# Kernel tuning notes

Measured on AMD Instinct MI355X. Metric: run time of the kernel, lower is better.

Reference implementation:

```python
import jax, jax.numpy as jnp
import numpy as np

NUM_SENSORS = 128
ANGLE = 0.5235987755982988  # 30 degrees
# delay_samples[s] = round(s * c/(2*fs) * sin(angle)/c * fs) = round(s*sin(angle)/2)

def _delay_samples(num_sensors):
    pos_scaled = np.arange(num_sensors) * np.sin(ANGLE) / 2.0
    return jnp.asarray(np.round(pos_scaled).astype(np.int32))


def setup_inputs() -> dict:
    key = jax.random.key(0)
    B, T, S = 16, 100000, NUM_SENSORS
    microphone_array = jax.random.normal(key, (B, T, S), dtype=jnp.float32)
    return {"microphone_array": microphone_array}


def reference(microphone_array):
    B, T, S = microphone_array.shape
    d = _delay_samples(S)                      # [S] int32, per-sensor shift
    t = jnp.arange(T, dtype=jnp.int32)
    idx = t[:, None] + d[None, :]              # [T, S] source sample index
    valid = idx < T                            # zero-pad past the end
    idx_c = jnp.minimum(idx, T - 1)
    # gather shifted signal per sensor: shifted[b, t, s] = x[b, t + d_s, s]
    gidx = jnp.broadcast_to(idx_c[None, :, :], (B, T, S))
    shifted = jnp.take_along_axis(microphone_array, gidx, axis=1)
    shifted = jnp.where(valid[None, :, :], shifted, jnp.zeros((), microphone_array.dtype))
    return jnp.sum(shifted, axis=-1) / S       # [B, T]
```

## Files before the change

### kernel.cpp

```cpp
#include <hip/hip_runtime.h>
#include <math.h>


#define SENS 128

#define FTT   224
#define FROWS (FTT + 32)
#define FRSTR (FTT + 2)
#define FNSLOT 33

__global__ __launch_bounds__(256, 5)
void das3_kernel(const float* __restrict__ x, float* __restrict__ out, int T) {
    __shared__ float P[FNSLOT * FRSTR];

    const int tid = threadIdx.x;
    const int b   = blockIdx.y;
    const int t0  = blockIdx.x * FTT;
    const int L   = tid & 31;
    const int rb  = tid >> 5;

    const int s0 = 4 * L - (L > 0);
    const float* __restrict__ xrow  = x + (size_t)b * (size_t)T * SENS + s0;
    const float* __restrict__ xlast = x + (size_t)b * (size_t)T * SENS + (SENS - 1);

    float* __restrict__ Pw  = P + L * FRSTR - L;
    float* __restrict__ PwE = P + 32 * FRSTR - 32;

    if (t0 + FROWS <= T) {
        #pragma unroll
        for (int bb = 0; bb < 4; ++bb) {
            float4 v[8];
            float  vl[8];
            #pragma unroll
            for (int k = 0; k < 8; ++k) {
                const int r = (bb * 8 + k) * 8 + rb;
                v[k] = *(const float4*)(xrow + (size_t)(t0 + r) * SENS);
            }
            if (L == 31) {
                #pragma unroll
                for (int k = 0; k < 8; ++k) {
                    const int r = (bb * 8 + k) * 8 + rb;
                    vl[k] = xlast[(size_t)(t0 + r) * SENS];
                }
            }
            #pragma unroll
            for (int k = 0; k < 8; ++k) {
                const int r = (bb * 8 + k) * 8 + rb;
                const float4 q = v[k];
                const float R = q.x + q.y + q.z + (L ? q.w : 0.0f);
                if (r >= L && r < L + FTT) Pw[r] = R;
                if (L == 31 && r >= 32)    PwE[r] = vl[k];
            }
        }
    } else {
        for (int i = tid; i < FNSLOT * FRSTR; i += 256) P[i] = 0.0f;
        __syncthreads();
        for (int sw = 0; sw < FROWS / 8; ++sw) {
            const int r = sw * 8 + rb;
            const int u = t0 + r;
            if (u < T) {
                const float4 q = *(const float4*)(xrow + (size_t)u * SENS);
                const float R = q.x + q.y + q.z + (L ? q.w : 0.0f);
                if (r >= L && r < L + FTT) Pw[r] = R;
                if (L == 31 && r >= 32)    PwE[r] = xlast[(size_t)u * SENS];
            }
        }
    }
    __syncthreads();

    const int t = t0 + tid;
    if (tid < FTT && t < T) {
        float acc = 0.0f;
        #pragma unroll
        for (int j = 0; j < FNSLOT; ++j)
            acc += P[j * FRSTR + tid];
        out[(size_t)b * T + t] = acc * (1.0f / SENS);
    }
}

#define TT   256
#define ROWS (TT + 32)
#define RSTR (ROWS + 1)
#define NSLOT 64

struct Tabs {
    int off[NSLOT];
    unsigned cm1, cm2, cm3;
};

__global__ __launch_bounds__(256)
void das2_kernel(const float* __restrict__ x, float* __restrict__ out,
                 Tabs tb, int T) {
    __shared__ float P[NSLOT * RSTR];

    const int tid = threadIdx.x;
    const int b   = blockIdx.y;
    const int t0  = blockIdx.x * TT;

    const int L = tid & 31;
    const bool c1 = (tb.cm1 >> L) & 1u;
    const bool c2 = (tb.cm2 >> L) & 1u;
    const bool c3 = (tb.cm3 >> L) & 1u;
    const int rb = tid >> 5;
    float* __restrict__ Pw = P + (2 * L) * RSTR;
    const float* __restrict__ xb = x + (size_t)b * (size_t)T * SENS + 4 * L;

    if (t0 + ROWS <= T) {
        #pragma unroll 4
        for (int sw = 0; sw < ROWS / 8; ++sw) {
            const int r = sw * 8 + rb;
            const float4 v = *(const float4*)(xb + (size_t)(t0 + r) * SENS);
            float a = v.x;
            a += c1 ? v.y : 0.0f;
            a += c2 ? v.z : 0.0f;
            a += c3 ? v.w : 0.0f;
            const float g = (c1 ? 0.0f : v.y) + (c2 ? 0.0f : v.z)
                          + (c3 ? 0.0f : v.w);
            Pw[r]        = a;
            Pw[RSTR + r] = g;
        }
    } else {
        for (int i = tid; i < NSLOT * RSTR; i += 256) P[i] = 0.0f;
        __syncthreads();
        for (int sw = 0; sw < ROWS / 8; ++sw) {
            const int r = sw * 8 + rb;
            const int u = t0 + r;
            if (u < T) {
                const float4 v = *(const float4*)(xb + (size_t)u * SENS);
                float a = v.x;
                a += c1 ? v.y : 0.0f;
                a += c2 ? v.z : 0.0f;
                a += c3 ? v.w : 0.0f;
                const float g = (c1 ? 0.0f : v.y) + (c2 ? 0.0f : v.z)
                              + (c3 ? 0.0f : v.w);
                Pw[r]        = a;
                Pw[RSTR + r] = g;
            }
        }
    }
    __syncthreads();

    const int t = t0 + tid;
    if (t < T) {
        float acc = 0.0f;
        #pragma unroll
        for (int j = 0; j < NSLOT; ++j)
            acc += P[tid + tb.off[j]];
        out[(size_t)b * T + t] = acc * (1.0f / SENS);
    }
}

extern "C" void kernel_launch(void* const* d_in, const int* in_sizes, int n_in,
                              void* d_out, int out_size, void* d_ws, size_t ws_size,
                              hipStream_t stream) {
    const float* x = (const float*)d_in[0];
    float* out = (float*)d_out;

    const int B = 16;
    const int T = in_sizes[0] / (B * SENS);

    int d[SENS];
    const double sv = sin(0.5235987755982988);
    for (int s = 0; s < SENS; ++s)
        d[s] = (int)rint((double)s * sv / 2.0);

    bool fast = true;
    for (int L = 0; L < 32; ++L) {
        if (d[4 * L + 0] != L || d[4 * L + 1] != L ||
            d[4 * L + 2] != L || d[4 * L + 3] != L + 1) { fast = false; break; }
    }

    if (fast) {
        dim3 grid((T + FTT - 1) / FTT, B);
        das3_kernel<<<grid, dim3(256), 0, stream>>>(x, out, T);
    } else {
        Tabs tb;
        tb.cm1 = tb.cm2 = tb.cm3 = 0u;
        for (int L = 0; L < 32; ++L) {
            const int d0 = d[4 * L + 0], d1 = d[4 * L + 1];
            const int d2 = d[4 * L + 2], d3 = d[4 * L + 3];
            if (d1 == d0) tb.cm1 |= 1u << L;
            if (d2 == d0) tb.cm2 |= 1u << L;
            if (d3 == d0) tb.cm3 |= 1u << L;
            tb.off[2 * L + 0] = (2 * L + 0) * RSTR + d0;
            tb.off[2 * L + 1] = (2 * L + 1) * RSTR + d3;
        }
        dim3 grid((T + TT - 1) / TT, B);
        das2_kernel<<<grid, dim3(256), 0, stream>>>(x, out, tb, T);
    }
}
```

Before: 1.007 ms.

## Use aligned float4 loads with split shared slots and XCD-aware block remap

Replaces the misaligned per-lane float4 loads (offset by one sensor, plus an extra scalar load for the last sensor) with aligned float4 loads. Each lane stores the sum of its first three sensors and its fourth sensor in two separate shared-memory slots at different shifts, giving 64 slots instead of 33. The grid is flattened and block indices are remapped so that consecutive blocks are spread across the eight chiplets in contiguous chunks. Loads get cheaper and the stray scalar loads disappear, at the cost of more shared memory, lower occupancy and a longer reduction loop.

```diff
diff --git a/kernel.cpp b/kernel.cpp
--- a/kernel.cpp
+++ b/kernel.cpp
@@ -4,65 +4,60 @@
 
 #define SENS 128
 
-#define FTT   224
-#define FROWS (FTT + 32)
-#define FRSTR (FTT + 2)
-#define FNSLOT 33
+#define FTT    224
+#define FROWS  256
+#define FSTR   225
+#define FNSLOT 64
 
-__global__ __launch_bounds__(256, 5)
-void das3_kernel(const float* __restrict__ x, float* __restrict__ out, int T) {
-    __shared__ float P[FNSLOT * FRSTR];
+__global__ __launch_bounds__(256)
+void das4_kernel(const float* __restrict__ x, float* __restrict__ out,
+                 int T, int nwgx) {
+    __shared__ float P[FNSLOT * FSTR];
+
+    const int lin = blockIdx.x;
+    const int q8  = (nwgx * 16) >> 3;
+    const int wid = (lin & 7) * q8 + (lin >> 3);
+    const int by  = wid / nwgx;
+    const int bx  = wid - by * nwgx;
 
     const int tid = threadIdx.x;
-    const int b   = blockIdx.y;
-    const int t0  = blockIdx.x * FTT;
+    const int t0  = bx * FTT;
     const int L   = tid & 31;
     const int rb  = tid >> 5;
 
-    const int s0 = 4 * L - (L > 0);
-    const float* __restrict__ xrow  = x + (size_t)b * (size_t)T * SENS + s0;
-    const float* __restrict__ xlast = x + (size_t)b * (size_t)T * SENS + (SENS - 1);
-
-    float* __restrict__ Pw  = P + L * FRSTR - L;
-    float* __restrict__ PwE = P + 32 * FRSTR - 32;
+    const float* __restrict__ xb = x + (size_t)by * (size_t)T * SENS + 4 * L;
+    float* __restrict__ PA = P + (2 * L) * FSTR - L;
+    float* __restrict__ PB = P + (2 * L + 1) * FSTR - L - 1;
 
     if (t0 + FROWS <= T) {
         #pragma unroll
-        for (int bb = 0; bb < 4; ++bb) {
-            float4 v[8];
-            float  vl[8];
+        for (int bb = 0; bb < 2; ++bb) {
+            float4 v[16];
             #pragma unroll
-            for (int k = 0; k < 8; ++k) {
-                const int r = (bb * 8 + k) * 8 + rb;
-                v[k] = *(const float4*)(xrow + (size_t)(t0 + r) * SENS);
-            }
-            if (L == 31) {
-                #pragma unroll
-                for (int k = 0; k < 8; ++k) {
-                    const int r = (bb * 8 + k) * 8 + rb;
-                    vl[k] = xlast[(size_t)(t0 + r) * SENS];
-                }
+            for (int k = 0; k < 16; ++k) {
+                const int r = bb * 128 + k * 8 + rb;
+                v[k] = *(const float4*)(xb + (size_t)(t0 + r) * SENS);
             }
             #pragma unroll
-            for (int k = 0; k < 8; ++k) {
-                const int r = (bb * 8 + k) * 8 + rb;
-                const float4 q = v[k];
-                const float R = q.x + q.y + q.z + (L ? q.w : 0.0f);
-                if (r >= L && r < L + FTT) Pw[r] = R;
-                if (L == 31 && r >= 32)    PwE[r] = vl[k];
+            for (int k = 0; k < 16; ++k) {
+                const int r = bb * 128 + k * 8 + rb;
+                const float4 qv = v[k];
+                const float A = qv.x + qv.y + qv.z;
+                if (r >= L && r < L + FTT)      PA[r] = A;
+                if (r >= L + 1 && r < L + FSTR) PB[r] = qv.w;
             }
         }
     } else {
-        for (int i = tid; i < FNSLOT * FRSTR; i += 256) P[i] = 0.0f;
+        for (int i = tid; i < FNSLOT * FSTR; i += 256) P[i] = 0.0f;
         __syncthreads();
         for (int sw = 0; sw < FROWS / 8; ++sw) {
             const int r = sw * 8 + rb;
             const int u = t0 + r;
             if (u < T) {
-                const float4 q = *(const float4*)(xrow + (size_t)u * SENS);
-                const float R = q.x + q.y + q.z + (L ? q.w : 0.0f);
-                if (r >= L && r < L + FTT) Pw[r] = R;
-                if (L == 31 && r >= 32)    PwE[r] = xlast[(size_t)u * SENS];
+                const float4 qv = *(const float4*)(xb + (size_t)u * SENS);
+                const float A = qv.x + qv.y + qv.z;
+                if (r >= L && r < L + FTT)      PA[r] = A;
+                if (r >= L + 1 && r < L + FSTR) PB[r] = qv.w;
             }
         }
     }
@@ -73,8 +68,8 @@
         float acc = 0.0f;
         #pragma unroll
         for (int j = 0; j < FNSLOT; ++j)
-            acc += P[j * FRSTR + tid];
-        out[(size_t)b * T + t] = acc * (1.0f / SENS);
+            acc += P[j * FSTR + tid];
+        out[(size_t)by * T + t] = acc * (1.0f / SENS);
     }
 }
 
@@ -171,8 +166,9 @@
     }
 
     if (fast) {
-        dim3 grid((T + FTT - 1) / FTT, B);
-        das3_kernel<<<grid, dim3(256), 0, stream>>>(x, out, T);
+        const int nwgx = (T + FTT - 1) / FTT;
+        dim3 grid(nwgx * B);
+        das4_kernel<<<grid, dim3(256), 0, stream>>>(x, out, T, nwgx);
     } else {
         Tabs tb;
         tb.cm1 = tb.cm2 = tb.cm3 = 0u;
```

Result: no change. 1.008 ms (+0.1%).
